# Optimization experiments

Measured on AMD Instinct MI355X. Metric: run time of the kernel, lower is better.

Reference implementation:

```python
import jax, jax.numpy as jnp
import numpy as np

B, S = 16, 256                     # batch, seq_len
CB, DB = 8, 256                    # control_bits, data_bits
IN_DIM = CB + DB                   # 264
OUT = DB                           # output_bits defaults to data_bits
H = 512                            # hidden_state_dim (LSTM controller)
M = 64                             # memory_content_size
R = 4                              # read heads
N = S                              # memory_addresses_size = -1 -> seq_len
_SPLITS = [R * M, R, M, 1, M, M, R, 1, 1, 3 * R]
XI = int(np.sum(_SPLITS))          # interface vector size = 471
_OFF = np.cumsum(_SPLITS)


def setup_inputs():
    ks = jax.random.split(jax.random.key(0), 6)
    sc = lambda k, shape: jax.random.normal(k, shape, jnp.float32) * 0.02
    return {
        "inputs": jax.random.normal(ks[0], (B, S, IN_DIM), jnp.float32),
        "Wx": sc(ks[1], (IN_DIM + R * M, 4 * H)),
        "Wh": sc(ks[2], (H, 4 * H)),
        "b_lstm": jnp.zeros((4 * H,), jnp.float32),
        "W_xi": sc(ks[3], (H, XI)),
        "b_xi": jnp.zeros((XI,), jnp.float32),
        "W_y": sc(ks[4], (H, OUT)),
        "W_r": sc(ks[5], (R * M, OUT)),
        "b_y": jnp.zeros((OUT,), jnp.float32),
    }


def _oneplus(x):
    return 1.0 + jax.nn.softplus(x)


def _content_weights(mem, keys, beta):
    # mem [B,N,M], keys [B,K,M], beta [B,K] -> softmax over N: [B,K,N]
    mem_n = mem / (jnp.linalg.norm(mem, axis=-1, keepdims=True) + 1e-6)
    key_n = keys / (jnp.linalg.norm(keys, axis=-1, keepdims=True) + 1e-6)
    sim = jnp.einsum('bkm,bnm->bkn', key_n, mem_n)
    return jax.nn.softmax(beta[..., None] * sim, axis=-1)


def _allocation(usage):
    # DNC paper allocation weighting via ascending usage sort
    idx = jnp.argsort(usage, axis=-1)
    u_s = jnp.take_along_axis(usage, idx, axis=-1)
    prod_excl = jnp.concatenate([jnp.ones_like(u_s[:, :1]), jnp.cumprod(u_s, axis=-1)[:, :-1]], axis=-1)
    a_s = (1.0 - u_s) * prod_excl
    inv = jnp.argsort(idx, axis=-1)
    return jnp.take_along_axis(a_s, inv, axis=-1)


def _dnc_forward(inputs, Wx, Wh, b_lstm, W_xi, b_xi, W_y, W_r_out, b_y):
    b = inputs.shape[0]
    eye = jnp.eye(N, dtype=inputs.dtype)

    def step(carry, x):
        h, c, mem, usage, link, prec, w_r, w_w, r_vec = carry
        # LSTM controller on [input, prev read vectors]
        ctrl_in = jnp.concatenate([x, r_vec.reshape(b, R * M)], axis=-1)
        gates = ctrl_in @ Wx + h @ Wh + b_lstm
        i_g, f_g, g_g, o_g = jnp.split(gates, 4, axis=-1)
        c = jax.nn.sigmoid(f_g) * c + jax.nn.sigmoid(i_g) * jnp.tanh(g_g)
        h = jax.nn.sigmoid(o_g) * jnp.tanh(c)

        # interface vector split
        xi = h @ W_xi + b_xi
        k_r = xi[:, :_OFF[0]].reshape(b, R, M)
        beta_r = _oneplus(xi[:, _OFF[0]:_OFF[1]])
        k_w = xi[:, _OFF[1]:_OFF[2]][:, None, :]
        beta_w = _oneplus(xi[:, _OFF[2]:_OFF[3]])
        erase = jax.nn.sigmoid(xi[:, _OFF[3]:_OFF[4]])
        w_vec = xi[:, _OFF[4]:_OFF[5]]
        free = jax.nn.sigmoid(xi[:, _OFF[5]:_OFF[6]])
        g_a = jax.nn.sigmoid(xi[:, _OFF[6]:_OFF[7]])
        g_w = jax.nn.sigmoid(xi[:, _OFF[7]:_OFF[8]])
        pi = jax.nn.softmax(xi[:, _OFF[8]:_OFF[9]].reshape(b, R, 3), axis=-1)

        # usage / allocation (content-free addressing)
        psi = jnp.prod(1.0 - free[:, :, None] * w_r, axis=1)           # [B,N]
        usage = (usage + w_w - usage * w_w) * psi
        alloc = _allocation(usage)

        # write weighting + memory scatter update
        c_w = _content_weights(mem, k_w, beta_w)[:, 0]                 # [B,N]
        w_w = g_w * (g_a * alloc + (1.0 - g_a) * c_w)
        mem = mem * (1.0 - w_w[:, :, None] * erase[:, None, :]) + w_w[:, :, None] * w_vec[:, None, :]

        # temporal linkage
        link = (1.0 - w_w[:, :, None] - w_w[:, None, :]) * link + w_w[:, :, None] * prec[:, None, :]
        link = link * (1.0 - eye)
        prec = (1.0 - jnp.sum(w_w, axis=-1, keepdims=True)) * prec + w_w

        # read weightings (backward / content / forward modes)
        fwd_w = jnp.einsum('bij,brj->bri', link, w_r)
        bwd_w = jnp.einsum('bji,brj->bri', link, w_r)
        c_r = _content_weights(mem, k_r, beta_r)                       # [B,R,N]
        w_r = pi[..., 0:1] * bwd_w + pi[..., 1:2] * c_r + pi[..., 2:3] * fwd_w
        r_vec = jnp.einsum('brn,bnm->brm', w_r, mem)                   # [B,R,M]

        y = h @ W_y + r_vec.reshape(b, R * M) @ W_r_out + b_y
        return (h, c, mem, usage, link, prec, w_r, w_w, r_vec), y

    z = jnp.zeros
    carry0 = (z((b, H)), z((b, H)), z((b, N, M)), z((b, N)), z((b, N, N)),
              z((b, N)), z((b, R, N)), z((b, N)), z((b, R, M)))
    _, ys = jax.lax.scan(step, carry0, jnp.swapaxes(inputs, 0, 1))
    return jnp.swapaxes(ys, 0, 1)                                      # [B,S,OUT]


def reference(inputs, Wx, Wh, b_lstm, W_xi, b_xi, W_y, W_r, b_y):
    return _dnc_forward(inputs, Wx, Wh, b_lstm, W_xi, b_xi, W_y, W_r, b_y)
```

## Files before the change

kernel.cpp:

```cpp
#include <hip/hip_runtime.h>
#include <cstddef>

#define DEV __device__ __forceinline__

constexpr int S_ = 256;
constexpr int NB = 256;
constexpr int NT = 256;


constexpr size_t bH    = 0;
constexpr size_t bC    = 1024;
constexpr size_t bXI   = 1536;
constexpr size_t bKNR  = 2048;
constexpr size_t bALC  = 2304;
constexpr size_t bCW   = 2560;
constexpr size_t bWW   = 2816;
constexpr size_t bNRM  = 3072;
constexpr size_t bUSG  = 3328;
constexpr size_t bRV   = 3584;
constexpr size_t bYH   = 3840;
constexpr size_t bSCL  = 4096;
constexpr size_t bPI   = 4128;
constexpr size_t bERS  = 4160;
constexpr size_t bWVC  = 4224;
constexpr size_t bPRC  = 4288;
constexpr size_t bWR   = 4800;
constexpr size_t bFWD  = 5824;
constexpr size_t bBWDP = 6848;
constexpr size_t bFLG  = 10944;
constexpr size_t bMEM  = 11456;
constexpr size_t bLNK  = 27840;
constexpr size_t PB    = 93376;
constexpr size_t WS_TOTAL = PB*16;

typedef unsigned long long u64_;
union F2U { u64_ u; float2 f; };
DEV float2 ld2_agt(const float* p){ F2U c; c.u=__hip_atomic_load((const u64_*)p,__ATOMIC_RELAXED,__HIP_MEMORY_SCOPE_AGENT); return c.f; }
DEV void   st2_agt(float* p, float2 v){ F2U c; c.f=v; __hip_atomic_store((u64_*)p,c.u,__ATOMIC_RELAXED,__HIP_MEMORY_SCOPE_AGENT); }
DEV float  ld_agt(const float* p){ return __hip_atomic_load((float*)p,__ATOMIC_RELAXED,__HIP_MEMORY_SCOPE_AGENT); }
DEV void   st_agt(float* p,float v){ __hip_atomic_store(p,v,__ATOMIC_RELAXED,__HIP_MEMORY_SCOPE_AGENT); }

DEV float sigm(float x){ return 1.0f/(1.0f+expf(-x)); }
DEV float oneplus_(float x){ float sp = (x>20.0f)? x : log1pf(expf(x)); return 1.0f+sp; }

DEV float wredsum(float v){
  #pragma unroll
  for (int o=32;o>0;o>>=1) v += __shfl_xor(v,o);
  return v;
}
DEV float hredsum32(float v){
  #pragma unroll
  for (int o=16;o>0;o>>=1) v += __shfl_xor(v,o);
  return v;
}
DEV float wredmax(float v){
  #pragma unroll
  for (int o=32;o>0;o>>=1) v = fmaxf(v,__shfl_xor(v,o));
  return v;
}
DEV float bredsum(float v, float* red){
  v = wredsum(v);
  if ((threadIdx.x&63)==0) red[threadIdx.x>>6]=v;
  __syncthreads();
  float r = red[0]+red[1]+red[2]+red[3];
  __syncthreads();
  return r;
}
DEV float bredmax(float v, float* red){
  v = wredmax(v);
  if ((threadIdx.x&63)==0) red[threadIdx.x>>6]=v;
  __syncthreads();
  float r = fmaxf(fmaxf(red[0],red[1]),fmaxf(red[2],red[3]));
  __syncthreads();
  return r;
}

DEV void cbar(float* wsb, unsigned ep, int ci){
  unsigned* flg = (unsigned*)(wsb + bFLG);
  __syncthreads();
  if (threadIdx.x < 64){
    if (threadIdx.x == 0)
      __hip_atomic_store(flg + (size_t)ci*32, ep, __ATOMIC_RELAXED, __HIP_MEMORY_SCOPE_AGENT);
    const int l = threadIdx.x;
    bool ok;
    do {
      unsigned v = (l<16) ? __hip_atomic_load(flg + (size_t)l*32,
                      __ATOMIC_RELAXED, __HIP_MEMORY_SCOPE_AGENT) : ep;
      ok = __all(v >= ep);
      if (!ok) __builtin_amdgcn_s_sleep(1);
    } while (!ok);
  }
  __syncthreads();
}

__global__ void k_zero(float* __restrict__ ws){
  size_t i = (size_t)blockIdx.x*blockDim.x + threadIdx.x;
  size_t st = (size_t)gridDim.x*blockDim.x;
  for (; i<WS_TOTAL; i+=st) ws[i]=0.0f;
}

__global__ __launch_bounds__(NT, 2) void k_dnc(
    const float* __restrict__ xin, const float* __restrict__ Wx,
    const float* __restrict__ Wh,  const float* __restrict__ bl,
    const float* __restrict__ Wxi, const float* __restrict__ bxi,
    const float* __restrict__ Wy,  const float* __restrict__ Wr,
    const float* __restrict__ by,  float* __restrict__ out,
    float* __restrict__ ws)
{
  __shared__ float smem[14336];
  const int tid  = threadIdx.x;
  const int bid  = blockIdx.x;
  const int lane = tid & 63, wv = tid >> 6;
  const int x  = bid & 7;
  const int q  = bid >> 3;
  const int s  = q & 1;
  const int ci = q >> 1;
  const int b  = x + (s<<3);
  float* wsb = ws + (size_t)b*PB;
  unsigned ep = 0;

  for (int t=0; t<S_; ++t){
    {
      float* sact = smem;
      float* sred = smem + 1040;
      float* gall = smem + 2064;
      float* ysum = smem + 2192;
      const float* hrd = wsb + bH + (size_t)(t&1)*512;
      float* hwr = wsb + bH + (size_t)((t+1)&1)*512;
      for (int e=tid; e<1032; e+=NT){
        float v;
        if (e < 264)      v = xin[((size_t)(b*256+t))*264 + e];
        else if (e < 520) v = ld_agt(wsb + bRV + (e-264));
        else              v = ld_agt(hrd + (e-520));
        sact[e] = v;
      }
      __syncthreads();
      if (t > 0){
        int ks2 = tid>>4, cc = tid&15;
        int yc = (ci<<4) + cc;
        float a = 0.f;
        const float* wp = Wr + (size_t)(ks2*16)*256 + yc;
        const float* rp = sact + 264 + ks2*16;
        #pragma unroll
        for (int k=0;k<16;++k) a = fmaf(rp[k], wp[(size_t)k*256], a);
        ysum[ks2*16 + cc] = a;
        __syncthreads();
        if (tid < 16){
          float sm = 0.f;
          #pragma unroll
          for (int p=0;p<16;++p) sm += ysum[p*16 + tid];
          int yc2 = (ci<<4) + tid;
          out[((size_t)(b*256 + (t-1)))*256 + yc2] = ld_agt(wsb+bYH+yc2) + sm;
        }
        __syncthreads();
      }
      {
        const int colq = tid & 31;
        const int ksA  = tid >> 5;
        const int g    = colq >> 3;
        const int col  = (g<<9) + (ci<<5) + ((colq&7)<<2);
        float4 acc; acc.x=0.f; acc.y=0.f; acc.z=0.f; acc.w=0.f;
        const float4* wp; const float* xp; int kn;
        if (ksA < 4){
          int k0 = ksA*130; kn = 130;
          wp = (const float4*)(Wx + (size_t)k0*2048 + col);
          xp = sact + k0;
        } else {
          int k0 = (ksA-4)*128; kn = 128;
          wp = (const float4*)(Wh + (size_t)k0*2048 + col);
          xp = sact + 520 + k0;
        }
        const int nch = (kn+7)>>3;
        float4 buf[8];
        #pragma unroll
        for (int i=0;i<8;++i){
          int kk = (i<kn)? i : kn-1;
          buf[i] = wp[(size_t)kk*512];
        }
        for (int c=0; c<nch; ++c){
          float4 nbuf[8];
          int nb0 = (c+1)<<3;
          #pragma unroll
          for (int i=0;i<8;++i){
            int kk = nb0+i; kk = (kk<kn)? kk : kn-1;
            nbuf[i] = wp[(size_t)kk*512];
          }
          int kb = c<<3;
          #pragma unroll
          for (int i=0;i<8;++i){
            float xv = (kb+i<kn)? xp[kb+i] : 0.f;
            acc.x=fmaf(buf[i].x,xv,acc.x); acc.y=fmaf(buf[i].y,xv,acc.y);
            acc.z=fmaf(buf[i].z,xv,acc.z); acc.w=fmaf(buf[i].w,xv,acc.w);
          }
          #pragma unroll
          for (int i=0;i<8;++i) buf[i]=nbuf[i];
        }
        *(float4*)(sred + ksA*128 + (colq<<2)) = acc;
      }
      __syncthreads();
      if (tid < 128){
        int gg = tid>>5, cc = (ci<<5) + (tid&31);
        float sm = bl[(gg<<9)+cc];
        #pragma unroll
        for (int p=0;p<8;++p) sm += sred[(p<<7) + tid];
        gall[tid] = sm;
      }
      __syncthreads();
      if (tid < 32){
        int j = (ci<<5) + tid;
        float gi=gall[tid], gf=gall[32+tid], gg2=gall[64+tid], go=gall[96+tid];
        float co = wsb[bC + j];
        float cn = sigm(gf)*co + sigm(gi)*tanhf(gg2);
        float hn = sigm(go)*tanhf(cn);
        wsb[bC + j] = cn;
        st_agt(hwr + j, hn);
      }
    }
    ep++; cbar(wsb, ep, ci);

    {
      float* shh = smem;
      float* sp  = smem + 512;
      float* syh = smem + 768;
      const float* hcur = wsb + bH + (size_t)((t+1)&1)*512;
      for (int e=tid; e<512; e+=NT) shh[e] = ld_agt(hcur + e);
      __syncthreads();
      const int nc = (ci<15) ? 30 : 21;
      if (tid < 240){
        int ks = tid/30, cc = tid%30;
        if (cc < nc){
          int col = ci*30 + cc;
          float a = 0.f;
          const float* wp = Wxi + (size_t)(ks*64)*471 + col;
          const float* hp = shh + ks*64;
          #pragma unroll 8
          for (int k=0;k<64;++k) a = fmaf(hp[k], wp[(size_t)k*471], a);
          sp[ks*30 + cc] = a;
        }
      }
      {
        int ks = tid>>4, cc = tid&15;
        int col = (ci<<4) + cc;
        float a = 0.f;
        const float* wp = Wy + (size_t)(ks*32)*256 + col;
        const float* hp = shh + ks*32;
        #pragma unroll 8
        for (int k=0;k<32;++k) a = fmaf(hp[k], wp[(size_t)k*256], a);
        syh[ks*16 + cc] = a;
      }
      __syncthreads();
      if (tid < nc){
        float sm = bxi[ci*30 + tid];
        #pragma unroll
        for (int p=0;p<8;++p) sm += sp[p*30 + tid];
        st_agt(wsb + bXI + ci*30 + tid, sm);
      }
      if (tid < 16){
        float sm = by[(ci<<4) + tid];
        #pragma unroll
        for (int p=0;p<16;++p) sm += syh[p*16 + tid];
        st_agt(wsb + bYH + (ci<<4) + tid, sm);
      }
    }
    ep++; cbar(wsb, ep, ci);

    if (ci == 0){
      float* xv = smem; float* uu = smem+512; float* sa = smem+768;
      float* sb = smem+1024; float* red = smem+1280;
      if (tid < 240){
        float2 v = ld2_agt(wsb + bXI + (tid<<1));
        xv[tid<<1]=v.x; xv[(tid<<1)+1]=v.y;
      }
      __syncthreads();
      int n = tid;
      float f0=sigm(xv[453]), f1=sigm(xv[454]), f2v=sigm(xv[455]), f3=sigm(xv[456]);
      const float* wrb = wsb + bWR;
      float psi=(1.f-f0*ld_agt(wrb+n))*(1.f-f1*ld_agt(wrb+256+n))
               *(1.f-f2v*ld_agt(wrb+512+n))*(1.f-f3*ld_agt(wrb+768+n));
      float uo=wsb[bUSG+n];
      float wwp=ld_agt(wsb+bWW+n);
      float un=(uo+wwp-uo*wwp)*psi;
      uu[n]=un; wsb[bUSG+n]=un;
      __syncthreads();
      int rk=0;
      #pragma unroll 8
      for (int j=0;j<256;++j){
        float uj=uu[j];
        rk += (uj<un)||(uj==un && j<n);
      }
      sa[rk]=un;
      __syncthreads();
      float* cur=sa; float* nxt=sb;
      for (int off=1;off<256;off<<=1){
        float v=cur[n]; if (n>=off) v*=cur[n-off];
        nxt[n]=v;
        __syncthreads();
        float* tmp=cur; cur=nxt; nxt=tmp;
      }
      float pe = rk ? cur[rk-1] : 1.f;
      float al = (1.f-un)*pe;
      st_agt(wsb+bALC+n, al);
      float sumA = bredsum(al, red);
      if (tid==0){
        st_agt(wsb+bSCL+0, sigm(xv[457]));
        st_agt(wsb+bSCL+1, sigm(xv[458]));
        st_agt(wsb+bSCL+2, sumA);
      }
      {
        int r=tid>>6, m=tid&63;
        float kv=xv[(r<<6)+m];
        float s2=wredsum(kv*kv);
        float br=oneplus_(xv[256+r]);
        st_agt(wsb+bKNR+tid, kv*br/(sqrtf(s2)+1e-6f));
      }
      if (tid<4){
        float p0=xv[459+tid*3], p1=xv[460+tid*3], p2=xv[461+tid*3];
        float mx=fmaxf(p0,fmaxf(p1,p2));
        float e0=expf(p0-mx), e1=expf(p1-mx), e2=expf(p2-mx);
        float sm=e0+e1+e2;
        st_agt(wsb+bPI+tid*3+0, e0/sm);
        st_agt(wsb+bPI+tid*3+1, e1/sm);
        st_agt(wsb+bPI+tid*3+2, e2/sm);
      }
      if (tid<64){
        st_agt(wsb+bERS+tid, sigm(xv[325+tid]));
        st_agt(wsb+bWVC+tid, xv[389+tid]);
      }
    } else if (ci == 1){
      float* knw=smem; float* sims=smem+64; float* red=smem+320;
      const int half = lane>>5, l32 = lane&31;
      if (wv==0){
        float kv=ld_agt(wsb+bXI+260+lane);
        float s2=wredsum(kv*kv);
        float bw_=oneplus_(ld_agt(wsb+bXI+324));
        knw[lane]=kv*bw_/(sqrtf(s2)+1e-6f);
      }
      __syncthreads();
      const float* memb=wsb+bMEM;
      for (int i2=0;i2<32;++i2){
        int n=(wv<<6)+(i2<<1)+half;
        float2 v=ld2_agt(memb+(n<<6)+(l32<<1));
        float d=hredsum32(v.x*knw[l32<<1]+v.y*knw[(l32<<1)+1]);
        if (l32==0) sims[n]=d/(sqrtf(ld_agt(wsb+bNRM+n))+1e-6f);
      }
      __syncthreads();
      float sv=sims[tid];
      float mx=bredmax(sv,red); float e=expf(sv-mx); float sm=bredsum(e,red);
      st_agt(wsb+bCW+tid, e/sm);
    } else if (ci == 2){
      for (int e=tid;e<4096;e+=NT) st_agt(wsb+bBWDP+e, 0.f);
    }
    ep++; cbar(wsb, ep, ci);

    {
      float* wwl   = smem;
      float* wrl   = smem + 256;
      float* fpart = smem + 320;
      float* sscl  = smem + 576;
      const int ri = ci<<4;
      if (tid < 3) sscl[tid] = ld_agt(wsb+bSCL+tid);
      __syncthreads();
      float ga = sscl[0], gw = sscl[1], sA = sscl[2];
      float sww = gw*(ga*sA + (1.f-ga));
      int j = tid;
      float wj = gw*(ga*ld_agt(wsb+bALC+j) + (1.f-ga)*ld_agt(wsb+bCW+j));
      wwl[j] = wj;
      if (ci == 1) st_agt(wsb+bWW+j, wj);
      float pj = ld_agt(wsb+bPRC + (size_t)(t&1)*256 + j);
      if (ci == 0) st_agt(wsb+bPRC + (size_t)((t+1)&1)*256 + j, (1.f-sww)*pj + wj);
      const float* wrb = wsb + bWR;
      float wr0=ld_agt(wrb+j), wr1=ld_agt(wrb+256+j),
            wr2=ld_agt(wrb+512+j), wr3=ld_agt(wrb+768+j);
      if (tid < 64) wrl[(tid>>4)*16 + (tid&15)] = ld_agt(wrb + ((size_t)(tid>>4)<<8) + ri + (tid&15));
      __syncthreads();
      float b0=0.f,b1=0.f,b2=0.f,b3=0.f;
      float* lrow = wsb + bLNK + (size_t)ri*256;
      for (int il=0; il<16; ++il){
        int irow = ri + il;
        float Lo = lrow[il*256 + j];
        float wi = wwl[irow];
        float Ln = (1.f - wi - wj)*Lo + wi*pj;
        if (irow == j) Ln = 0.f;
        lrow[il*256 + j] = Ln;
        float s0=wredsum(Ln*wr0), s1=wredsum(Ln*wr1), s2=wredsum(Ln*wr2), s3=wredsum(Ln*wr3);
        if (lane==0){
          fpart[wv*64 + il]      = s0;
          fpart[wv*64 + 16 + il] = s1;
          fpart[wv*64 + 32 + il] = s2;
          fpart[wv*64 + 48 + il] = s3;
        }
        b0=fmaf(Ln, wrl[il],    b0);
        b1=fmaf(Ln, wrl[16+il], b1);
        b2=fmaf(Ln, wrl[32+il], b2);
        b3=fmaf(Ln, wrl[48+il], b3);
      }
      __syncthreads();
      if (tid < 64){
        int r = tid>>4, il = tid&15;
        float sm = fpart[r*16+il] + fpart[64+r*16+il] + fpart[128+r*16+il] + fpart[192+r*16+il];
        st_agt(wsb+bFWD + ((size_t)r<<8) + ri + il, sm);
      }
      float* slot = wsb + bBWDP + (size_t)(ci&3)*1024;
      atomicAdd(&slot[j], b0);      atomicAdd(&slot[256+j], b1);
      atomicAdd(&slot[512+j], b2);  atomicAdd(&slot[768+j], b3);
      {
        int row2 = tid>>5, c2 = tid&31;
        float2 er  = ld2_agt(wsb+bERS + (c2<<1));
        float2 wv2 = ld2_agt(wsb+bWVC + (c2<<1));
        #pragma unroll
        for (int it=0; it<2; ++it){
          int row = ri + row2 + it*8;
          float wwn = wwl[row];
          float2 v = ld2_agt(wsb+bMEM + ((size_t)row<<6) + (c2<<1));
          v.x = v.x*(1.f - wwn*er.x) + wwn*wv2.x;
          v.y = v.y*(1.f - wwn*er.y) + wwn*wv2.y;
          st2_agt(wsb+bMEM + ((size_t)row<<6) + (c2<<1), v);
          float s2 = hredsum32(v.x*v.x + v.y*v.y);
          if (c2==0) st_agt(wsb+bNRM+row, s2);
        }
      }
    }
    ep++; cbar(wsb, ep, ci);

    if (ci < 4){
      int r = ci;
      float* knl=smem; float* sims=smem+64; float* wrs=smem+320;
      float* part=smem+576; float* red=smem+832;
      if (wv==0) knl[lane]=ld_agt(wsb+bKNR+(r<<6)+lane);
      __syncthreads();
      const float* memb = wsb + bMEM;
      {
        int row2 = tid>>5, c2 = tid&31;
        for (int it=0; it<32; ++it){
          int n = row2 + it*8;
          float2 v = ld2_agt(memb + ((size_t)n<<6) + (c2<<1));
          float d = hredsum32(v.x*knl[c2<<1] + v.y*knl[(c2<<1)+1]);
          if (c2==0) sims[n] = d/(sqrtf(ld_agt(wsb+bNRM+n))+1e-6f);
        }
      }
      __syncthreads();
      float sv=sims[tid];
      float mx=bredmax(sv,red); float e=expf(sv-mx); float sm=bredsum(e,red);
      float cr=e/sm;
      float p0=ld_agt(wsb+bPI+r*3), p1=ld_agt(wsb+bPI+r*3+1), p2=ld_agt(wsb+bPI+r*3+2);
      float bwv = ld_agt(wsb+bBWDP + ((size_t)r<<8) + tid)
                + ld_agt(wsb+bBWDP + 1024 + ((size_t)r<<8) + tid)
                + ld_agt(wsb+bBWDP + 2048 + ((size_t)r<<8) + tid)
                + ld_agt(wsb+bBWDP + 3072 + ((size_t)r<<8) + tid);
      float wr = p0*bwv + p1*cr + p2*ld_agt(wsb+bFWD+((size_t)r<<8)+tid);
      st_agt(wsb+bWR+((size_t)r<<8)+tid, wr);
      wrs[tid]=wr;
      __syncthreads();
      {
        int m = tid&63, ksn = tid>>6;
        float a=0.f;
        #pragma unroll 8
        for (int n0=0;n0<64;++n0){
          int n = (ksn<<6)+n0;
          a = fmaf(wrs[n], ld_agt(memb + ((size_t)n<<6) + m), a);
        }
        part[(ksn<<6)+m]=a;
      }
      __syncthreads();
      if (tid<64)
        st_agt(wsb+bRV+(r<<6)+tid, part[tid]+part[64+tid]+part[128+tid]+part[192+tid]);
    }
    ep++; cbar(wsb, ep, ci);
  }

  {
    float* srv  = smem;
    float* ysum = smem + 256;
    for (int e=tid;e<256;e+=NT) srv[e]=ld_agt(wsb+bRV+e);
    __syncthreads();
    int ks2 = tid>>4, cc = tid&15;
    int yc = (ci<<4) + cc;
    float a = 0.f;
    const float* wp = Wr + (size_t)(ks2*16)*256 + yc;
    const float* rp = srv + ks2*16;
    #pragma unroll
    for (int k=0;k<16;++k) a = fmaf(rp[k], wp[(size_t)k*256], a);
    ysum[ks2*16 + cc] = a;
    __syncthreads();
    if (tid < 16){
      float sm = 0.f;
      #pragma unroll
      for (int p=0;p<16;++p) sm += ysum[p*16 + tid];
      int yc2 = (ci<<4) + tid;
      out[((size_t)(b*256 + 255))*256 + yc2] = ld_agt(wsb+bYH+yc2) + sm;
    }
  }
}

extern "C" void kernel_launch(void* const* d_in, const int* in_sizes, int n_in,
                              void* d_out, int out_size, void* d_ws, size_t ws_size,
                              hipStream_t stream) {
  (void)in_sizes; (void)out_size;
  if (n_in < 9) return;
  const float* xin = (const float*)d_in[0];
  const float* Wx  = (const float*)d_in[1];
  const float* Wh  = (const float*)d_in[2];
  const float* bl  = (const float*)d_in[3];
  const float* Wxi = (const float*)d_in[4];
  const float* bxi = (const float*)d_in[5];
  const float* Wy  = (const float*)d_in[6];
  const float* Wr  = (const float*)d_in[7];
  const float* by  = (const float*)d_in[8];
  float* out = (float*)d_out;
  float* ws  = (float*)d_ws;
  if (ws_size < WS_TOTAL*sizeof(float)) return;

  hipLaunchKernelGGL(k_zero, dim3(512), dim3(256), 0, stream, ws);
  hipLaunchKernelGGL(k_dnc, dim3(NB), dim3(NT), 0, stream,
                     xin, Wx, Wh, bl, Wxi, bxi, Wy, Wr, by, out, ws);
}
```

Measured before the change: 23.33 ms.

## Double block size to 512 threads and split per-step work across more threads

Raises the block size from 256 to 512 threads and halves the K-split chunk per thread in the LSTM gate GEMV, the interface/output GEMVs, the similarity scan and the read-vector reduction. In the link-update phase, the memory erase/write now runs on the upper 256 threads at the same time as the link matrix update on the lower 256. The goal is to shorten the serial per-timestep critical path of this latency-bound recurrent kernel. In exchange, launch bounds drop to one block per CU, there are more partial sums to reduce, and several phases leave half the threads idle.

```diff
diff --git a/kernel.cpp b/kernel.cpp
--- a/kernel.cpp
+++ b/kernel.cpp
@@ -5,7 +5,7 @@
 
 constexpr int S_ = 256;
 constexpr int NB = 256;
-constexpr int NT = 256;
+constexpr int NT = 512;
 
 
 constexpr size_t bH    = 0;
@@ -58,19 +58,21 @@
   for (int o=32;o>0;o>>=1) v = fmaxf(v,__shfl_xor(v,o));
   return v;
 }
-DEV float bredsum(float v, float* red){
+DEV float bredsum512(float v, float* red){
   v = wredsum(v);
   if ((threadIdx.x&63)==0) red[threadIdx.x>>6]=v;
   __syncthreads();
-  float r = red[0]+red[1]+red[2]+red[3];
+  float r = red[0]+red[1]+red[2]+red[3]+red[4]+red[5]+red[6]+red[7];
   __syncthreads();
   return r;
 }
-DEV float bredmax(float v, float* red){
+DEV float bredmax512(float v, float* red){
   v = wredmax(v);
   if ((threadIdx.x&63)==0) red[threadIdx.x>>6]=v;
   __syncthreads();
-  float r = fmaxf(fmaxf(red[0],red[1]),fmaxf(red[2],red[3]));
+  float r = red[0];
+  #pragma unroll
+  for (int i=1;i<8;++i) r = fmaxf(r, red[i]);
   __syncthreads();
   return r;
 }
@@ -99,7 +101,7 @@
   for (; i<WS_TOTAL; i+=st) ws[i]=0.0f;
 }
 
-__global__ __launch_bounds__(NT, 2) void k_dnc(
+__global__ __launch_bounds__(NT, 1) void k_dnc(
     const float* __restrict__ xin, const float* __restrict__ Wx,
     const float* __restrict__ Wh,  const float* __restrict__ bl,
     const float* __restrict__ Wxi, const float* __restrict__ bxi,
@@ -107,7 +109,7 @@
     const float* __restrict__ by,  float* __restrict__ out,
     float* __restrict__ ws)
 {
-  __shared__ float smem[14336];
+  __shared__ float smem[20736];
   const int tid  = threadIdx.x;
   const int bid  = blockIdx.x;
   const int lane = tid & 63, wv = tid >> 6;
@@ -123,8 +125,8 @@
     {
       float* sact = smem;
       float* sred = smem + 1040;
-      float* gall = smem + 2064;
-      float* ysum = smem + 2192;
+      float* gall = smem + 3088;
+      float* ysum = smem + 3216;
       const float* hrd = wsb + bH + (size_t)(t&1)*512;
       float* hwr = wsb + bH + (size_t)((t+1)&1)*512;
       for (int e=tid; e<1032; e+=NT){
@@ -136,14 +138,16 @@
       }
       __syncthreads();
       if (t > 0){
-        int ks2 = tid>>4, cc = tid&15;
-        int yc = (ci<<4) + cc;
-        float a = 0.f;
-        const float* wp = Wr + (size_t)(ks2*16)*256 + yc;
-        const float* rp = sact + 264 + ks2*16;
-        #pragma unroll
-        for (int k=0;k<16;++k) a = fmaf(rp[k], wp[(size_t)k*256], a);
-        ysum[ks2*16 + cc] = a;
+        if (tid < 256){
+          int ks2 = tid>>4, cc = tid&15;
+          int yc = (ci<<4) + cc;
+          float a = 0.f;
+          const float* wp = Wr + (size_t)(ks2*16)*256 + yc;
+          const float* rp = sact + 264 + ks2*16;
+          #pragma unroll
+          for (int k=0;k<16;++k) a = fmaf(rp[k], wp[(size_t)k*256], a);
+          ysum[ks2*16 + cc] = a;
+        }
         __syncthreads();
         if (tid < 16){
           float sm = 0.f;
@@ -157,16 +161,16 @@
       {
         const int colq = tid & 31;
         const int ksA  = tid >> 5;
-        const int g    = colq >> 3;
-        const int col  = (g<<9) + (ci<<5) + ((colq&7)<<2);
+        const int g2   = colq >> 3;
+        const int col  = (g2<<9) + (ci<<5) + ((colq&7)<<2);
         float4 acc; acc.x=0.f; acc.y=0.f; acc.z=0.f; acc.w=0.f;
         const float4* wp; const float* xp; int kn;
-        if (ksA < 4){
-          int k0 = ksA*130; kn = 130;
+        if (ksA < 8){
+          int k0 = ksA*65; kn = 65;
           wp = (const float4*)(Wx + (size_t)k0*2048 + col);
           xp = sact + k0;
         } else {
-          int k0 = (ksA-4)*128; kn = 128;
+          int k0 = (ksA-8)*64; kn = 64;
           wp = (const float4*)(Wh + (size_t)k0*2048 + col);
           xp = sact + 520 + k0;
         }
@@ -202,7 +206,7 @@
         int gg = tid>>5, cc = (ci<<5) + (tid&31);
         float sm = bl[(gg<<9)+cc];
         #pragma unroll
-        for (int p=0;p<8;++p) sm += sred[(p<<7) + tid];
+        for (int p=0;p<16;++p) sm += sred[(p<<7) + tid];
         gall[tid] = sm;
       }
       __syncthreads();
@@ -221,20 +225,20 @@
     {
       float* shh = smem;
       float* sp  = smem + 512;
-      float* syh = smem + 768;
+      float* syh = smem + 1024;
       const float* hcur = wsb + bH + (size_t)((t+1)&1)*512;
-      for (int e=tid; e<512; e+=NT) shh[e] = ld_agt(hcur + e);
+      if (tid < 512) shh[tid] = ld_agt(hcur + tid);
       __syncthreads();
       const int nc = (ci<15) ? 30 : 21;
-      if (tid < 240){
+      if (tid < 480){
         int ks = tid/30, cc = tid%30;
         if (cc < nc){
           int col = ci*30 + cc;
           float a = 0.f;
-          const float* wp = Wxi + (size_t)(ks*64)*471 + col;
-          const float* hp = shh + ks*64;
+          const float* wp = Wxi + (size_t)(ks*32)*471 + col;
+          const float* hp = shh + ks*32;
           #pragma unroll 8
-          for (int k=0;k<64;++k) a = fmaf(hp[k], wp[(size_t)k*471], a);
+          for (int k=0;k<32;++k) a = fmaf(hp[k], wp[(size_t)k*471], a);
           sp[ks*30 + cc] = a;
         }
       }
@@ -242,23 +246,23 @@
         int ks = tid>>4, cc = tid&15;
         int col = (ci<<4) + cc;
         float a = 0.f;
-        const float* wp = Wy + (size_t)(ks*32)*256 + col;
-        const float* hp = shh + ks*32;
+        const float* wp = Wy + (size_t)(ks*16)*256 + col;
+        const float* hp = shh + ks*16;
         #pragma unroll 8
-        for (int k=0;k<32;++k) a = fmaf(hp[k], wp[(size_t)k*256], a);
+        for (int k=0;k<16;++k) a = fmaf(hp[k], wp[(size_t)k*256], a);
         syh[ks*16 + cc] = a;
       }
       __syncthreads();
       if (tid < nc){
         float sm = bxi[ci*30 + tid];
         #pragma unroll
-        for (int p=0;p<8;++p) sm += sp[p*30 + tid];
+        for (int p=0;p<16;++p) sm += sp[p*30 + tid];
         st_agt(wsb + bXI + ci*30 + tid, sm);
       }
       if (tid < 16){
         float sm = by[(ci<<4) + tid];
         #pragma unroll
-        for (int p=0;p<16;++p) sm += syh[p*16 + tid];
+        for (int p=0;p<32;++p) sm += syh[p*16 + tid];
         st_agt(wsb + bYH + (ci<<4) + tid, sm);
       }
     }
@@ -267,46 +271,57 @@
     if (ci == 0){
       float* xv = smem; float* uu = smem+512; float* sa = smem+768;
       float* sb = smem+1024; float* red = smem+1280;
+      const bool act = tid < 256;
       if (tid < 240){
         float2 v = ld2_agt(wsb + bXI + (tid<<1));
         xv[tid<<1]=v.x; xv[(tid<<1)+1]=v.y;
       }
       __syncthreads();
       int n = tid;
-      float f0=sigm(xv[453]), f1=sigm(xv[454]), f2v=sigm(xv[455]), f3=sigm(xv[456]);
-      const float* wrb = wsb + bWR;
-      float psi=(1.f-f0*ld_agt(wrb+n))*(1.f-f1*ld_agt(wrb+256+n))
-               *(1.f-f2v*ld_agt(wrb+512+n))*(1.f-f3*ld_agt(wrb+768+n));
-      float uo=wsb[bUSG+n];
-      float wwp=ld_agt(wsb+bWW+n);
-      float un=(uo+wwp-uo*wwp)*psi;
-      uu[n]=un; wsb[bUSG+n]=un;
+      float un = 0.f;
+      if (act){
+        float f0=sigm(xv[453]), f1=sigm(xv[454]), f2v=sigm(xv[455]), f3=sigm(xv[456]);
+        const float* wrb = wsb + bWR;
+        float psi=(1.f-f0*ld_agt(wrb+n))*(1.f-f1*ld_agt(wrb+256+n))
+                 *(1.f-f2v*ld_agt(wrb+512+n))*(1.f-f3*ld_agt(wrb+768+n));
+        float uo=wsb[bUSG+n];
+        float wwp=ld_agt(wsb+bWW+n);
+        un=(uo+wwp-uo*wwp)*psi;
+        uu[n]=un; wsb[bUSG+n]=un;
+      }
       __syncthreads();
       int rk=0;
-      #pragma unroll 8
-      for (int j=0;j<256;++j){
-        float uj=uu[j];
-        rk += (uj<un)||(uj==un && j<n);
-      }
-      sa[rk]=un;
+      if (act){
+        #pragma unroll 8
+        for (int j=0;j<256;++j){
+          float uj=uu[j];
+          rk += (uj<un)||(uj==un && j<n);
+        }
+        sa[rk]=un;
+      }
       __syncthreads();
       float* cur=sa; float* nxt=sb;
       for (int off=1;off<256;off<<=1){
-        float v=cur[n]; if (n>=off) v*=cur[n-off];
-        nxt[n]=v;
+        if (act){
+          float v=cur[n]; if (n>=off) v*=cur[n-off];
+          nxt[n]=v;
+        }
         __syncthreads();
         float* tmp=cur; cur=nxt; nxt=tmp;
       }
-      float pe = rk ? cur[rk-1] : 1.f;
-      float al = (1.f-un)*pe;
-      st_agt(wsb+bALC+n, al);
-      float sumA = bredsum(al, red);
+      float al = 0.f;
+      if (act){
+        float pe = rk ? cur[rk-1] : 1.f;
+        al = (1.f-un)*pe;
+        st_agt(wsb+bALC+n, al);
+      }
+      float sumA = bredsum512(act? al : 0.f, red);
       if (tid==0){
         st_agt(wsb+bSCL+0, sigm(xv[457]));
         st_agt(wsb+bSCL+1, sigm(xv[458]));
         st_agt(wsb+bSCL+2, sumA);
       }
-      {
+      if (act){
         int r=tid>>6, m=tid&63;
         float kv=xv[(r<<6)+m];
         float s2=wredsum(kv*kv);
@@ -328,7 +343,6 @@
       }
     } else if (ci == 1){
       float* knw=smem; float* sims=smem+64; float* red=smem+320;
-      const int half = lane>>5, l32 = lane&31;
       if (wv==0){
         float kv=ld_agt(wsb+bXI+260+lane);
         float s2=wredsum(kv*kv);
@@ -337,16 +351,21 @@
       }
       __syncthreads();
       const float* memb=wsb+bMEM;
-      for (int i2=0;i2<32;++i2){
-        int n=(wv<<6)+(i2<<1)+half;
-        float2 v=ld2_agt(memb+(n<<6)+(l32<<1));
-        float d=hredsum32(v.x*knw[l32<<1]+v.y*knw[(l32<<1)+1]);
-        if (l32==0) sims[n]=d/(sqrtf(ld_agt(wsb+bNRM+n))+1e-6f);
-      }
-      __syncthreads();
-      float sv=sims[tid];
-      float mx=bredmax(sv,red); float e=expf(sv-mx); float sm=bredsum(e,red);
-      st_agt(wsb+bCW+tid, e/sm);
+      {
+        int hw = tid>>5, c2 = tid&31;
+        for (int it=0; it<16; ++it){
+          int n = (hw<<4) + it;
+          float2 v=ld2_agt(memb+((size_t)n<<6)+(c2<<1));
+          float d=hredsum32(v.x*knw[c2<<1]+v.y*knw[(c2<<1)+1]);
+          if (c2==0) sims[n]=d/(sqrtf(ld_agt(wsb+bNRM+n))+1e-6f);
+        }
+      }
+      __syncthreads();
+      float sv = (tid<256)? sims[tid] : -1e30f;
+      float mx=bredmax512(sv,red);
+      float e = (tid<256)? expf(sv-mx) : 0.f;
+      float sm=bredsum512(e,red);
+      if (tid<256) st_agt(wsb+bCW+tid, e/sm);
     } else if (ci == 2){
       for (int e=tid;e<4096;e+=NT) st_agt(wsb+bBWDP+e, 0.f);
     }
@@ -355,56 +374,56 @@
     {
       float* wwl   = smem;
       float* wrl   = smem + 256;
-      float* fpart = smem + 320;
-      float* sscl  = smem + 576;
+      float* fpart = smem + 512;
+      float* sscl  = smem + 784;
       const int ri = ci<<4;
       if (tid < 3) sscl[tid] = ld_agt(wsb+bSCL+tid);
       __syncthreads();
       float ga = sscl[0], gw = sscl[1], sA = sscl[2];
       float sww = gw*(ga*sA + (1.f-ga));
-      int j = tid;
-      float wj = gw*(ga*ld_agt(wsb+bALC+j) + (1.f-ga)*ld_agt(wsb+bCW+j));
-      wwl[j] = wj;
-      if (ci == 1) st_agt(wsb+bWW+j, wj);
-      float pj = ld_agt(wsb+bPRC + (size_t)(t&1)*256 + j);
-      if (ci == 0) st_agt(wsb+bPRC + (size_t)((t+1)&1)*256 + j, (1.f-sww)*pj + wj);
-      const float* wrb = wsb + bWR;
-      float wr0=ld_agt(wrb+j), wr1=ld_agt(wrb+256+j),
-            wr2=ld_agt(wrb+512+j), wr3=ld_agt(wrb+768+j);
-      if (tid < 64) wrl[(tid>>4)*16 + (tid&15)] = ld_agt(wrb + ((size_t)(tid>>4)<<8) + ri + (tid&15));
-      __syncthreads();
-      float b0=0.f,b1=0.f,b2=0.f,b3=0.f;
-      float* lrow = wsb + bLNK + (size_t)ri*256;
-      for (int il=0; il<16; ++il){
-        int irow = ri + il;
-        float Lo = lrow[il*256 + j];
-        float wi = wwl[irow];
-        float Ln = (1.f - wi - wj)*Lo + wi*pj;
-        if (irow == j) Ln = 0.f;
-        lrow[il*256 + j] = Ln;
-        float s0=wredsum(Ln*wr0), s1=wredsum(Ln*wr1), s2=wredsum(Ln*wr2), s3=wredsum(Ln*wr3);
-        if (lane==0){
-          fpart[wv*64 + il]      = s0;
-          fpart[wv*64 + 16 + il] = s1;
-          fpart[wv*64 + 32 + il] = s2;
-          fpart[wv*64 + 48 + il] = s3;
-        }
-        b0=fmaf(Ln, wrl[il],    b0);
-        b1=fmaf(Ln, wrl[16+il], b1);
-        b2=fmaf(Ln, wrl[32+il], b2);
-        b3=fmaf(Ln, wrl[48+il], b3);
-      }
-      __syncthreads();
-      if (tid < 64){
-        int r = tid>>4, il = tid&15;
-        float sm = fpart[r*16+il] + fpart[64+r*16+il] + fpart[128+r*16+il] + fpart[192+r*16+il];
-        st_agt(wsb+bFWD + ((size_t)r<<8) + ri + il, sm);
-      }
-      float* slot = wsb + bBWDP + (size_t)(ci&3)*1024;
-      atomicAdd(&slot[j], b0);      atomicAdd(&slot[256+j], b1);
-      atomicAdd(&slot[512+j], b2);  atomicAdd(&slot[768+j], b3);
-      {
-        int row2 = tid>>5, c2 = tid&31;
+      float wj=0.f, pj=0.f, wr0=0.f, wr1=0.f, wr2=0.f, wr3=0.f;
+      if (tid < 256){
+        int j = tid;
+        wj = gw*(ga*ld_agt(wsb+bALC+j) + (1.f-ga)*ld_agt(wsb+bCW+j));
+        wwl[j] = wj;
+        if (ci == 1) st_agt(wsb+bWW+j, wj);
+        pj = ld_agt(wsb+bPRC + (size_t)(t&1)*256 + j);
+        if (ci == 0) st_agt(wsb+bPRC + (size_t)((t+1)&1)*256 + j, (1.f-sww)*pj + wj);
+        const float* wrb = wsb + bWR;
+        wr0=ld_agt(wrb+j); wr1=ld_agt(wrb+256+j);
+        wr2=ld_agt(wrb+512+j); wr3=ld_agt(wrb+768+j);
+        if (tid < 64) wrl[(tid>>4)*16 + (tid&15)] = ld_agt(wrb + ((size_t)(tid>>4)<<8) + ri + (tid&15));
+      }
+      __syncthreads();
+      if (tid < 256){
+        int j = tid;
+        float b0=0.f,b1=0.f,b2=0.f,b3=0.f;
+        float* lrow = wsb + bLNK + (size_t)ri*256;
+        for (int il=0; il<16; ++il){
+          int irow = ri + il;
+          float Lo = lrow[il*256 + j];
+          float wi = wwl[irow];
+          float Ln = (1.f - wi - wj)*Lo + wi*pj;
+          if (irow == j) Ln = 0.f;
+          lrow[il*256 + j] = Ln;
+          float s0=wredsum(Ln*wr0), s1=wredsum(Ln*wr1), s2=wredsum(Ln*wr2), s3=wredsum(Ln*wr3);
+          if (lane==0){
+            fpart[wv*64 + il]      = s0;
+            fpart[wv*64 + 16 + il] = s1;
+            fpart[wv*64 + 32 + il] = s2;
+            fpart[wv*64 + 48 + il] = s3;
+          }
+          b0=fmaf(Ln, wrl[il],    b0);
+          b1=fmaf(Ln, wrl[16+il], b1);
+          b2=fmaf(Ln, wrl[32+il], b2);
+          b3=fmaf(Ln, wrl[48+il], b3);
+        }
+        float* slot = wsb + bBWDP + (size_t)(ci&3)*1024;
+        atomicAdd(&slot[j], b0);      atomicAdd(&slot[256+j], b1);
+        atomicAdd(&slot[512+j], b2);  atomicAdd(&slot[768+j], b3);
+      } else {
+        int t2 = tid-256;
+        int row2 = t2>>5, c2 = t2&31;
         float2 er  = ld2_agt(wsb+bERS + (c2<<1));
         float2 wv2 = ld2_agt(wsb+bWVC + (c2<<1));
         #pragma unroll
@@ -419,51 +438,65 @@
           if (c2==0) st_agt(wsb+bNRM+row, s2);
         }
       }
+      __syncthreads();
+      if (tid < 64){
+        int r = tid>>4, il = tid&15;
+        float sm = fpart[r*16+il] + fpart[64+r*16+il] + fpart[128+r*16+il] + fpart[192+r*16+il];
+        st_agt(wsb+bFWD + ((size_t)r<<8) + ri + il, sm);
+      }
     }
     ep++; cbar(wsb, ep, ci);
 
     if (ci < 4){
       int r = ci;
       float* knl=smem; float* sims=smem+64; float* wrs=smem+320;
-      float* part=smem+576; float* red=smem+832;
+      float* part=smem+576; float* red=smem+1088;
       if (wv==0) knl[lane]=ld_agt(wsb+bKNR+(r<<6)+lane);
       __syncthreads();
       const float* memb = wsb + bMEM;
       {
-        int row2 = tid>>5, c2 = tid&31;
-        for (int it=0; it<32; ++it){
-          int n = row2 + it*8;
+        int hw = tid>>5, c2 = tid&31;
+        for (int it=0; it<16; ++it){
+          int n = (hw<<4) + it;
           float2 v = ld2_agt(memb + ((size_t)n<<6) + (c2<<1));
           float d = hredsum32(v.x*knl[c2<<1] + v.y*knl[(c2<<1)+1]);
           if (c2==0) sims[n] = d/(sqrtf(ld_agt(wsb+bNRM+n))+1e-6f);
         }
       }
       __syncthreads();
-      float sv=sims[tid];
-      float mx=bredmax(sv,red); float e=expf(sv-mx); float sm=bredsum(e,red);
-      float cr=e/sm;
-      float p0=ld_agt(wsb+bPI+r*3), p1=ld_agt(wsb+bPI+r*3+1), p2=ld_agt(wsb+bPI+r*3+2);
-      float bwv = ld_agt(wsb+bBWDP + ((size_t)r<<8) + tid)
-                + ld_agt(wsb+bBWDP + 1024 + ((size_t)r<<8) + tid)
-                + ld_agt(wsb+bBWDP + 2048 + ((size_t)r<<8) + tid)
-                + ld_agt(wsb+bBWDP + 3072 + ((size_t)r<<8) + tid);
-      float wr = p0*bwv + p1*cr + p2*ld_agt(wsb+bFWD+((size_t)r<<8)+tid);
-      st_agt(wsb+bWR+((size_t)r<<8)+tid, wr);
-      wrs[tid]=wr;
+      float sv = (tid<256)? sims[tid] : -1e30f;
+      float mx=bredmax512(sv,red);
+      float e = (tid<256)? expf(sv-mx) : 0.f;
+      float sm=bredsum512(e,red);
+      if (tid < 256){
+        float cr=e/sm;
+        float p0=ld_agt(wsb+bPI+r*3), p1=ld_agt(wsb+bPI+r*3+1), p2=ld_agt(wsb+bPI+r*3+2);
+        float bwv = ld_agt(wsb+bBWDP + ((size_t)r<<8) + tid)
+                  + ld_agt(wsb+bBWDP + 1024 + ((size_t)r<<8) + tid)
+                  + ld_agt(wsb+bBWDP + 2048 + ((size_t)r<<8) + tid)
+                  + ld_agt(wsb+bBWDP + 3072 + ((size_t)r<<8) + tid);
+        float wr = p0*bwv + p1*cr + p2*ld_agt(wsb+bFWD+((size_t)r<<8)+tid);
+        st_agt(wsb+bWR+((size_t)r<<8)+tid, wr);
+        wrs[tid]=wr;
+      }
       __syncthreads();
       {
         int m = tid&63, ksn = tid>>6;
         float a=0.f;
         #pragma unroll 8
-        for (int n0=0;n0<64;++n0){
-          int n = (ksn<<6)+n0;
+        for (int n0=0;n0<32;++n0){
+          int n = (ksn<<5)+n0;
           a = fmaf(wrs[n], ld_agt(memb + ((size_t)n<<6) + m), a);
         }
         part[(ksn<<6)+m]=a;
       }
       __syncthreads();
-      if (tid<64)
-        st_agt(wsb+bRV+(r<<6)+tid, part[tid]+part[64+tid]+part[128+tid]+part[192+tid]);
+      if (tid<64){
+        float sm2=0.f;
+        #pragma unroll
+        for (int p=0;p<8;++p) sm2 += part[(p<<6)+tid];
+        st_agt(wsb+bRV+(r<<6)+tid, sm2);
+      }
     }
     ep++; cbar(wsb, ep, ci);
   }
@@ -471,16 +504,18 @@
   {
     float* srv  = smem;
     float* ysum = smem + 256;
-    for (int e=tid;e<256;e+=NT) srv[e]=ld_agt(wsb+bRV+e);
+    if (tid < 256) srv[tid]=ld_agt(wsb+bRV+tid);
     __syncthreads();
-    int ks2 = tid>>4, cc = tid&15;
-    int yc = (ci<<4) + cc;
-    float a = 0.f;
-    const float* wp = Wr + (size_t)(ks2*16)*256 + yc;
-    const float* rp = srv + ks2*16;
-    #pragma unroll
-    for (int k=0;k<16;++k) a = fmaf(rp[k], wp[(size_t)k*256], a);
-    ysum[ks2*16 + cc] = a;
+    if (tid < 256){
+      int ks2 = tid>>4, cc = tid&15;
+      int yc = (ci<<4) + cc;
+      float a = 0.f;
+      const float* wp = Wr + (size_t)(ks2*16)*256 + yc;
+      const float* rp = srv + ks2*16;
+      #pragma unroll
+      for (int k=0;k<16;++k) a = fmaf(rp[k], wp[(size_t)k*256], a);
+      ysum[ks2*16 + cc] = a;
+    }
     __syncthreads();
     if (tid < 16){
       float sm = 0.f;
```

After: 25.05 ms. 7.4% more time.

## Redistribute LSTM gate GEMV across blocks with cross-batch step flags

Applied to the files above, without the earlier changes.

Splits the LSTM gate computation differently: each block now computes 4 gate column groups of 32 for a different batch element (gb=ci), publishing the results to a shared gate buffer with a counter, instead of computing all four gates for its own column slice with float4 loads. Per-batch step flags and gate counters synchronize the producers and consumers, and several agent-scope atomics become system-scope. The aim is a different weight-access pattern and better spreading of gate work. In exchange it adds spin-waits, loses the float4 vectorized, prefetched loads, and system-scope atomics may be slower.

```diff
diff --git a/kernel.cpp b/kernel.cpp
--- a/kernel.cpp
+++ b/kernel.cpp
@@ -30,7 +30,10 @@
 constexpr size_t bFLG  = 10944;
 constexpr size_t bMEM  = 11456;
 constexpr size_t bLNK  = 27840;
-constexpr size_t PB    = 93376;
+constexpr size_t bGT   = 93376;
+constexpr size_t bGCT  = 95424;
+constexpr size_t bSTF  = 95456;
+constexpr size_t PB    = 95488;
 constexpr size_t WS_TOTAL = PB*16;
 
 typedef unsigned long long u64_;
@@ -39,6 +42,8 @@
 DEV void   st2_agt(float* p, float2 v){ F2U c; c.f=v; __hip_atomic_store((u64_*)p,c.u,__ATOMIC_RELAXED,__HIP_MEMORY_SCOPE_AGENT); }
 DEV float  ld_agt(const float* p){ return __hip_atomic_load((float*)p,__ATOMIC_RELAXED,__HIP_MEMORY_SCOPE_AGENT); }
 DEV void   st_agt(float* p,float v){ __hip_atomic_store(p,v,__ATOMIC_RELAXED,__HIP_MEMORY_SCOPE_AGENT); }
+DEV float  ld_sys(const float* p){ return __hip_atomic_load((float*)p,__ATOMIC_RELAXED,__HIP_MEMORY_SCOPE_SYSTEM); }
+DEV void   st_sys(float* p,float v){ __hip_atomic_store(p,v,__ATOMIC_RELAXED,__HIP_MEMORY_SCOPE_SYSTEM); }
 
 DEV float sigm(float x){ return 1.0f/(1.0f+expf(-x)); }
 DEV float oneplus_(float x){ float sp = (x>20.0f)? x : log1pf(expf(x)); return 1.0f+sp; }
@@ -117,30 +122,71 @@
   const int ci = q >> 1;
   const int b  = x + (s<<3);
   float* wsb = ws + (size_t)b*PB;
+  const int gb = ci;
+  const int gh = s;
+  float* wsg = ws + (size_t)gb*PB;
   unsigned ep = 0;
 
   for (int t=0; t<S_; ++t){
     {
+      unsigned* stf = (unsigned*)(wsg + bSTF);
+      if (tid==0){
+        while (__hip_atomic_load(stf, __ATOMIC_RELAXED, __HIP_MEMORY_SCOPE_SYSTEM) < (unsigned)t)
+          __builtin_amdgcn_s_sleep(1);
+      }
+      __syncthreads();
       float* sact = smem;
       float* sred = smem + 1040;
-      float* gall = smem + 2064;
-      float* ysum = smem + 2192;
-      const float* hrd = wsb + bH + (size_t)(t&1)*512;
-      float* hwr = wsb + bH + (size_t)((t+1)&1)*512;
+      const float* hrd = wsg + bH + (size_t)(t&1)*512;
       for (int e=tid; e<1032; e+=NT){
         float v;
-        if (e < 264)      v = xin[((size_t)(b*256+t))*264 + e];
-        else if (e < 520) v = ld_agt(wsb + bRV + (e-264));
-        else              v = ld_agt(hrd + (e-520));
+        if (e < 264)      v = xin[((size_t)(gb*256+t))*264 + e];
+        else if (e < 520) v = ld_sys(wsg + bRV + (e-264));
+        else              v = ld_sys(hrd + (e-520));
         sact[e] = v;
       }
       __syncthreads();
+      const int ks = tid>>5, c = tid&31;
+      for (int j=0;j<4;++j){
+        int g   = x + ((gh*4 + j)<<3);
+        int col = (g<<5) + c;
+        float a = 0.f;
+        {
+          const float* wp = Wx + (size_t)(ks*65)*2048 + col;
+          const float* xp = sact + ks*65;
+          #pragma unroll 8
+          for (int k=0;k<65;++k) a = fmaf(xp[k], wp[(size_t)k*2048], a);
+        }
+        {
+          const float* wp = Wh + (size_t)(ks*64)*2048 + col;
+          const float* xp = sact + 520 + ks*64;
+          #pragma unroll 8
+          for (int k=0;k<64;++k) a = fmaf(xp[k], wp[(size_t)k*2048], a);
+        }
+        sred[ks*32 + c] = a;
+        __syncthreads();
+        if (tid < 32){
+          float sm = bl[(g<<5) + tid];
+          #pragma unroll
+          for (int p=0;p<8;++p) sm += sred[p*32 + tid];
+          st_sys(wsg + bGT + (g<<5) + tid, sm);
+        }
+        __syncthreads();
+      }
+      if (tid==0) atomicAdd((unsigned*)(wsg + bGCT), 1u);
+    }
+
+    {
+      float* srv  = smem;
+      float* ysum = smem + 256;
       if (t > 0){
+        for (int e=tid;e<256;e+=NT) srv[e]=ld_sys(wsb+bRV+e);
+        __syncthreads();
         int ks2 = tid>>4, cc = tid&15;
         int yc = (ci<<4) + cc;
         float a = 0.f;
         const float* wp = Wr + (size_t)(ks2*16)*256 + yc;
-        const float* rp = sact + 264 + ks2*16;
+        const float* rp = srv + ks2*16;
         #pragma unroll
         for (int k=0;k<16;++k) a = fmaf(rp[k], wp[(size_t)k*256], a);
         ysum[ks2*16 + cc] = a;
@@ -154,66 +200,23 @@
         }
         __syncthreads();
       }
-      {
-        const int colq = tid & 31;
-        const int ksA  = tid >> 5;
-        const int g    = colq >> 3;
-        const int col  = (g<<9) + (ci<<5) + ((colq&7)<<2);
-        float4 acc; acc.x=0.f; acc.y=0.f; acc.z=0.f; acc.w=0.f;
-        const float4* wp; const float* xp; int kn;
-        if (ksA < 4){
-          int k0 = ksA*130; kn = 130;
-          wp = (const float4*)(Wx + (size_t)k0*2048 + col);
-          xp = sact + k0;
-        } else {
-          int k0 = (ksA-4)*128; kn = 128;
-          wp = (const float4*)(Wh + (size_t)k0*2048 + col);
-          xp = sact + 520 + k0;
-        }
-        const int nch = (kn+7)>>3;
-        float4 buf[8];
-        #pragma unroll
-        for (int i=0;i<8;++i){
-          int kk = (i<kn)? i : kn-1;
-          buf[i] = wp[(size_t)kk*512];
-        }
-        for (int c=0; c<nch; ++c){
-          float4 nbuf[8];
-          int nb0 = (c+1)<<3;
-          #pragma unroll
-          for (int i=0;i<8;++i){
-            int kk = nb0+i; kk = (kk<kn)? kk : kn-1;
-            nbuf[i] = wp[(size_t)kk*512];
-          }
-          int kb = c<<3;
-          #pragma unroll
-          for (int i=0;i<8;++i){
-            float xv = (kb+i<kn)? xp[kb+i] : 0.f;
-            acc.x=fmaf(buf[i].x,xv,acc.x); acc.y=fmaf(buf[i].y,xv,acc.y);
-            acc.z=fmaf(buf[i].z,xv,acc.z); acc.w=fmaf(buf[i].w,xv,acc.w);
-          }
-          #pragma unroll
-          for (int i=0;i<8;++i) buf[i]=nbuf[i];
-        }
-        *(float4*)(sred + ksA*128 + (colq<<2)) = acc;
-      }
-      __syncthreads();
-      if (tid < 128){
-        int gg = tid>>5, cc = (ci<<5) + (tid&31);
-        float sm = bl[(gg<<9)+cc];
-        #pragma unroll
-        for (int p=0;p<8;++p) sm += sred[(p<<7) + tid];
-        gall[tid] = sm;
+      unsigned* gct = (unsigned*)(wsb + bGCT);
+      if (tid==0){
+        while (__hip_atomic_load(gct, __ATOMIC_RELAXED, __HIP_MEMORY_SCOPE_SYSTEM) < 16u*(unsigned)(t+1))
+          __builtin_amdgcn_s_sleep(1);
       }
       __syncthreads();
       if (tid < 32){
         int j = (ci<<5) + tid;
-        float gi=gall[tid], gf=gall[32+tid], gg2=gall[64+tid], go=gall[96+tid];
+        float gi = ld_sys(wsb+bGT+j);
+        float gf = ld_sys(wsb+bGT+512+j);
+        float gg2= ld_sys(wsb+bGT+1024+j);
+        float go = ld_sys(wsb+bGT+1536+j);
         float co = wsb[bC + j];
         float cn = sigm(gf)*co + sigm(gi)*tanhf(gg2);
         float hn = sigm(go)*tanhf(cn);
         wsb[bC + j] = cn;
-        st_agt(hwr + j, hn);
+        st_sys(wsb + bH + (size_t)((t+1)&1)*512 + j, hn);
       }
     }
     ep++; cbar(wsb, ep, ci);
@@ -223,7 +226,7 @@
       float* sp  = smem + 512;
       float* syh = smem + 768;
       const float* hcur = wsb + bH + (size_t)((t+1)&1)*512;
-      for (int e=tid; e<512; e+=NT) shh[e] = ld_agt(hcur + e);
+      for (int e=tid; e<512; e+=NT) shh[e] = ld_sys(hcur + e);
       __syncthreads();
       const int nc = (ci<15) ? 30 : 21;
       if (tid < 240){
@@ -463,15 +466,19 @@
       }
       __syncthreads();
       if (tid<64)
-        st_agt(wsb+bRV+(r<<6)+tid, part[tid]+part[64+tid]+part[128+tid]+part[192+tid]);
+        st_sys(wsb+bRV+(r<<6)+tid, part[tid]+part[64+tid]+part[128+tid]+part[192+tid]);
     }
     ep++; cbar(wsb, ep, ci);
+
+    if (ci==0 && tid==0)
+      __hip_atomic_store((unsigned*)(wsb + bSTF), (unsigned)(t+1),
+                         __ATOMIC_RELAXED, __HIP_MEMORY_SCOPE_SYSTEM);
   }
 
   {
     float* srv  = smem;
     float* ysum = smem + 256;
-    for (int e=tid;e<256;e+=NT) srv[e]=ld_agt(wsb+bRV+e);
+    for (int e=tid;e<256;e+=NT) srv[e]=ld_sys(wsb+bRV+e);
     __syncthreads();
     int ks2 = tid>>4, cc = tid&15;
     int yc = (ci<<4) + cc;
```

New measurement: 25.18 ms. 7.9% more time.
